# Kernel tuning notes

Hardware: AMD Instinct MI355X
Metric: run time of the kernel (lower is better)

## Reference

```python
import jax, jax.numpy as jnp
import numpy as np

N_NODES = 100000
N_EDGES = 800000
IN_DIM = 128
HIDDEN = 128
CLASSES = 40


def _glorot(key, shape):
    fan_in, fan_out = shape
    lim = (6.0 / (fan_in + fan_out)) ** 0.5
    return jax.random.uniform(key, shape, jnp.float32, -lim, lim)


def setup_inputs() -> dict:
    key = jax.random.key(0)
    ks = jax.random.split(key, 8)
    x = jax.random.normal(ks[0], (N_NODES, IN_DIM), jnp.float32)
    edge_index = jax.random.randint(ks[1], (2, N_EDGES), 0, N_NODES, jnp.int64)
    # SAGEConv layer 1: lin_l (neighbor, with bias), lin_r (root, no bias)
    W1_l = _glorot(ks[2], (IN_DIM, HIDDEN))
    W1_r = _glorot(ks[3], (IN_DIM, HIDDEN))
    b1 = jnp.zeros((HIDDEN,), jnp.float32)
    # SAGEConv layer 2
    W2_l = _glorot(ks[4], (HIDDEN, CLASSES))
    W2_r = _glorot(ks[5], (HIDDEN, CLASSES))
    b2 = jnp.zeros((CLASSES,), jnp.float32)
    return {"x": x, "edge_index": edge_index, "W1_l": W1_l, "W1_r": W1_r,
            "b1": b1, "W2_l": W2_l, "W2_r": W2_r, "b2": b2}


def _sage_conv(x, src, dst, W_l, W_r, b):
    # mean aggregation of source-node features into destination nodes
    msgs = x[src]                                             # [E, d] gather
    agg = jax.ops.segment_sum(msgs, dst, num_segments=N_NODES)  # [N, d]
    cnt = jax.ops.segment_sum(jnp.ones((src.shape[0],), x.dtype), dst,
                              num_segments=N_NODES)           # [N]
    mean = agg / jnp.maximum(cnt, 1.0)[:, None]
    return mean @ W_l + x @ W_r + b


def reference(x, edge_index, W1_l, W1_r, b1, W2_l, W2_r, b2):
    src, dst = edge_index[0], edge_index[1]
    h = _sage_conv(x, src, dst, W1_l, W1_r, b1)
    h = jax.nn.relu(h)
    # F.dropout in eval mode is the identity (deterministic reference)
    out = _sage_conv(h, src, dst, W2_l, W2_r, b2)
    return out
```

## Files before the change

### kernel.cpp

```cpp
#include <hip/hip_runtime.h>
#include <hip/hip_bf16.h>

#define N_NODES 100000
#define N_EDGES 800000
#define IN_DIM  128
#define HIDDEN  128
#define CLASSES 40
#define CAP     32
#define NSH     8
#define SLICES  100
#define EPB     8000
#define BIN_B   (NSH*SLICES)
#define CAST_B  12500
#define PACK_B  24
#define CUR_STRIDE 12544

typedef __attribute__((ext_vector_type(8))) short bf16x8;
typedef __attribute__((ext_vector_type(4))) float floatx4;

__device__ __forceinline__ float bf2f(unsigned short u) {
    return __uint_as_float(((unsigned int)u) << 16);
}
__device__ __forceinline__ unsigned short f2bf(float f) {
    unsigned int u = __float_as_uint(f);
    unsigned int r = 0x7fffu + ((u >> 16) & 1u);
    return (unsigned short)((u + r) >> 16);
}
__device__ __forceinline__ int curIdx(int d) { return (d & 7) * CUR_STRIDE + (d >> 3); }

__global__ void k_prep(const int* __restrict__ src, const int* __restrict__ dst,
                       int* __restrict__ cur, int* __restrict__ csr,
                       const float* __restrict__ x, unsigned short* __restrict__ A1,
                       const float* __restrict__ W1l, const float* __restrict__ W1r,
                       unsigned short* __restrict__ Bp1,
                       const float* __restrict__ W2l, const float* __restrict__ W2r,
                       unsigned short* __restrict__ Bp2) {
    int blk = blockIdx.x;
    if (blk < BIN_B) {
        int g = blk & 7;
        int slice = blk >> 3;
        const int4* s4p = reinterpret_cast<const int4*>(src) + slice * (EPB / 4);
        const int4* d4p = reinterpret_cast<const int4*>(dst) + slice * (EPB / 4);
        for (int i = threadIdx.x; i < EPB / 4; i += 256) {
            int4 d4 = d4p[i];
            int4 s4 = s4p[i];
            #pragma unroll
            for (int j = 0; j < 4; ++j) {
                int d = (&d4.x)[j];
                if ((d & 7) == g) {
                    int s = (&s4.x)[j];
                    int slot = atomicAdd(&cur[g * CUR_STRIDE + (d >> 3)], 1);
                    if (slot < CAP) csr[d * CAP + slot] = s;
                }
            }
        }
    } else if (blk < BIN_B + CAST_B) {
        int t = (blk - BIN_B) * 256 + threadIdx.x;
        int n = t >> 5, g = t & 31;
        float4 v = reinterpret_cast<const float4*>(x + (size_t)n * 128)[g];
        ushort4 u = { f2bf(v.x), f2bf(v.y), f2bf(v.z), f2bf(v.w) };
        *(ushort4*)(A1 + (size_t)n * 256 + 128 + g * 4) = u;
    } else {
        int t = (blk - BIN_B - CAST_B) * 256 + threadIdx.x;
        if (t < 4096) {
            int o = t >> 7, n = t & 127;
            const float* W = (o < 16) ? W1l : W1r;
            int k0 = (o & 15) * 8;
            union { unsigned short us[8]; uint4 v; } pk;
            #pragma unroll
            for (int j = 0; j < 8; ++j) pk.us[j] = f2bf(W[(size_t)(k0 + j) * 128 + n]);
            *(uint4*)(Bp1 + (size_t)t * 8) = pk.v;
        } else {
            int t2 = t - 4096;
            int o = t2 >> 7, n = t2 & 127;
            const float* W = (n < 64) ? W2l : W2r;
            int col = n & 63;
            int k0 = o * 8;
            union { unsigned short us[8]; uint4 v; } pk;
            #pragma unroll
            for (int j = 0; j < 8; ++j)
                pk.us[j] = (col < 40) ? f2bf(W[(size_t)(k0 + j) * 40 + col]) : (unsigned short)0;
            *(uint4*)(Bp2 + (size_t)t2 * 8) = pk.v;
        }
    }
}

__global__ __launch_bounds__(256)
void k_fused(unsigned short* __restrict__ A1, float* __restrict__ Rbuf,
             const int* __restrict__ deg, const int* __restrict__ csr,
             const unsigned short* __restrict__ Bp1, const float* __restrict__ b1,
             const unsigned short* __restrict__ Bp2) {
    __shared__ unsigned short S[4][16][136];
    int wv = threadIdx.x >> 6, lane = threadIdx.x & 63;
    int q = lane >> 4, nn = lane & 15;
    int m0 = blockIdx.x * 64 + wv * 16;

    for (int i = 0; i < 16; i += 2) {
        int nA = m0 + i, nB = m0 + i + 1;
        int aA = min(nA, N_NODES - 1), aB = min(nB, N_NODES - 1);
        int cntA = (nA < N_NODES) ? min(deg[curIdx(aA)], CAP) : 0;
        int cntB = (nB < N_NODES) ? min(deg[curIdx(aB)], CAP) : 0;
        int nl = csr[(lane < 32 ? aA : aB) * CAP + (lane & 31)];
        float accA[8] = {}, accB[8] = {};
        int mx = max(cntA, cntB);
        for (int b = 0; b < mx; b += 16) {
            #pragma unroll
            for (int u = 0; u < 4; ++u) {
                int e = b + u * 4 + q;
                int iA = min(e, cntA - 1) & 31;
                int iB = min(e, cntB - 1) & 31;
                int sA = __shfl(nl, iA, 64);
                int sB = __shfl(nl, 32 + iB, 64);
                bf16x8 vA = {}, vB = {};
                if (e < cntA) vA = *(const bf16x8*)(A1 + (size_t)sA * 256 + 128 + nn * 8);
                if (e < cntB) vB = *(const bf16x8*)(A1 + (size_t)sB * 256 + 128 + nn * 8);
                #pragma unroll
                for (int j = 0; j < 8; ++j) {
                    accA[j] += bf2f((unsigned short)vA[j]);
                    accB[j] += bf2f((unsigned short)vB[j]);
                }
            }
        }
        #pragma unroll
        for (int j = 0; j < 8; ++j) {
            accA[j] += __shfl_xor(accA[j], 16, 64);
            accA[j] += __shfl_xor(accA[j], 32, 64);
            accB[j] += __shfl_xor(accB[j], 16, 64);
            accB[j] += __shfl_xor(accB[j], 32, 64);
        }
        if (lane < 16) {
            float invA = 1.0f / fmaxf((float)cntA, 1.0f);
            float invB = 1.0f / fmaxf((float)cntB, 1.0f);
            union { unsigned short us[8]; bf16x8 v; } pA, pB;
            #pragma unroll
            for (int j = 0; j < 8; ++j) {
                pA.us[j] = f2bf(accA[j] * invA);
                pB.us[j] = f2bf(accB[j] * invB);
            }
            *(bf16x8*)(&S[wv][i][lane * 8])     = pA.v;
            *(bf16x8*)(&S[wv][i + 1][lane * 8]) = pB.v;
        }
    }

    int ma = m0 + nn;
    bool mv = (ma < N_NODES);
    const unsigned short* arow = A1 + (size_t)ma * 256;

    floatx4 acc[8] = {};
    #pragma unroll
    for (int kt = 0; kt < 8; ++kt) {
        bf16x8 a;
        if (kt < 4) {
            a = *(const bf16x8*)(&S[wv][nn][kt * 32 + q * 8]);
        } else {
            a = bf16x8{};
            if (mv) a = *(const bf16x8*)(arow + kt * 32 + q * 8);
        }
        bf16x8 b[8];
        #pragma unroll
        for (int nt = 0; nt < 8; ++nt)
            b[nt] = *(const bf16x8*)(Bp1 + ((size_t)((kt * 4 + q) * 128 + nt * 16 + nn)) * 8);
        #pragma unroll
        for (int nt = 0; nt < 8; ++nt)
            acc[nt] = __builtin_amdgcn_mfma_f32_16x16x32_bf16(a, b[nt], acc[nt], 0, 0, 0);
    }
    #pragma unroll
    for (int nt = 0; nt < 8; ++nt) {
        int col = nt * 16 + nn;
        float bias = b1[col];
        #pragma unroll
        for (int r = 0; r < 4; ++r)
            S[wv][q * 4 + r][col] = f2bf(fmaxf(acc[nt][r] + bias, 0.f));
    }
    floatx4 acc2[8] = {};
    #pragma unroll
    for (int kt = 0; kt < 4; ++kt) {
        bf16x8 a = *(const bf16x8*)(&S[wv][nn][kt * 32 + q * 8]);
        bf16x8 b[8];
        #pragma unroll
        for (int nt = 0; nt < 8; ++nt)
            b[nt] = *(const bf16x8*)(Bp2 + ((size_t)((kt * 4 + q) * 128 + nt * 16 + nn)) * 8);
        #pragma unroll
        for (int nt = 0; nt < 8; ++nt)
            acc2[nt] = __builtin_amdgcn_mfma_f32_16x16x32_bf16(a, b[nt], acc2[nt], 0, 0, 0);
    }
    #pragma unroll
    for (int nt = 0; nt < 4; ++nt) {
        int col = nt * 16 + nn;
        #pragma unroll
        for (int r = 0; r < 4; ++r) {
            int ro = m0 + q * 4 + r;
            if (ro < N_NODES)
                A1[(size_t)ro * 256 + col] = f2bf(acc2[nt][r]);
        }
    }
    #pragma unroll
    for (int nt = 4; nt < 8; ++nt) {
        int col = (nt - 4) * 16 + nn;
        #pragma unroll
        for (int r = 0; r < 4; ++r) {
            int ro = m0 + q * 4 + r;
            if (ro < N_NODES)
                Rbuf[(size_t)ro * 64 + col] = acc2[nt][r];
        }
    }
}

__global__ void k_agg2(const unsigned short* __restrict__ A1, const float* __restrict__ Rbuf,
                       const int* __restrict__ deg, const int* __restrict__ csr,
                       const float* __restrict__ b2, float* __restrict__ out) {
    int pair = blockIdx.x * 4 + (threadIdx.x >> 6);
    int nA = pair * 2, nB = nA + 1;
    int lane = threadIdx.x & 63;
    if (nA >= N_NODES) return;
    int aB = min(nB, N_NODES - 1);
    int cntA = min(deg[curIdx(nA)], CAP);
    int cntB = (nB < N_NODES) ? min(deg[curIdx(aB)], CAP) : 0;
    int nl = csr[(lane < 32 ? nA : aB) * CAP + (lane & 31)];
    int r = lane >> 3, c = lane & 7;
    float accA[8] = {}, accB[8] = {};
    int mx = max(cntA, cntB);
    for (int b = 0; b < mx; b += 16) {
        #pragma unroll
        for (int u = 0; u < 2; ++u) {
            int e = b + u * 8 + r;
            int sA = __shfl(nl, min(e, cntA - 1) & 31, 64);
            int sB = __shfl(nl, 32 + (min(e, cntB - 1) & 31), 64);
            bf16x8 vA = {}, vB = {};
            if (e < cntA) vA = *(const bf16x8*)(A1 + (size_t)sA * 256 + c * 8);
            if (e < cntB) vB = *(const bf16x8*)(A1 + (size_t)sB * 256 + c * 8);
            #pragma unroll
            for (int j = 0; j < 8; ++j) {
                accA[j] += bf2f((unsigned short)vA[j]);
                accB[j] += bf2f((unsigned short)vB[j]);
            }
        }
    }
    #pragma unroll
    for (int j = 0; j < 8; ++j) {
        accA[j] += __shfl_xor(accA[j], 8, 64);
        accA[j] += __shfl_xor(accA[j], 16, 64);
        accA[j] += __shfl_xor(accA[j], 32, 64);
        accB[j] += __shfl_xor(accB[j], 8, 64);
        accB[j] += __shfl_xor(accB[j], 16, 64);
        accB[j] += __shfl_xor(accB[j], 32, 64);
    }
    if (lane < 5) {
        float invA = 1.0f / fmaxf((float)cntA, 1.0f);
        const float* RrowA = Rbuf + (size_t)nA * 64;
        float o[8];
        #pragma unroll
        for (int j = 0; j < 8; ++j)
            o[j] = accA[j] * invA + RrowA[c * 8 + j] + b2[c * 8 + j];
        float* opA = out + (size_t)nA * CLASSES + c * 8;
        *(float4*)(opA)     = make_float4(o[0], o[1], o[2], o[3]);
        *(float4*)(opA + 4) = make_float4(o[4], o[5], o[6], o[7]);
        if (nB < N_NODES) {
            float invB = 1.0f / fmaxf((float)cntB, 1.0f);
            const float* RrowB = Rbuf + (size_t)nB * 64;
            #pragma unroll
            for (int j = 0; j < 8; ++j)
                o[j] = accB[j] * invB + RrowB[c * 8 + j] + b2[c * 8 + j];
            float* opB = out + (size_t)nB * CLASSES + c * 8;
            *(float4*)(opB)     = make_float4(o[0], o[1], o[2], o[3]);
            *(float4*)(opB + 4) = make_float4(o[4], o[5], o[6], o[7]);
        }
    }
}

extern "C" void kernel_launch(void* const* d_in, const int* in_sizes, int n_in,
                              void* d_out, int out_size, void* d_ws, size_t ws_size,
                              hipStream_t stream) {
    const float* x   = (const float*)d_in[0];
    const int*   ei  = (const int*)d_in[1];
    const float* W1l = (const float*)d_in[2];
    const float* W1r = (const float*)d_in[3];
    const float* b1  = (const float*)d_in[4];
    const float* W2l = (const float*)d_in[5];
    const float* W2r = (const float*)d_in[6];
    const float* b2  = (const float*)d_in[7];
    float* out = (float*)d_out;

    const int* src = ei;
    const int* dst = ei + N_EDGES;

    char* ws = (char*)d_ws;
    size_t off = 0;
    auto alloc = [&](size_t bytes) { void* p = ws + off; off += (bytes + 511) & ~(size_t)511; return p; };
    int* cur = (int*)alloc((size_t)NSH * CUR_STRIDE * 4);
    int* csr = (int*)alloc((size_t)N_NODES * CAP * 4);
    unsigned short* Bp1 = (unsigned short*)alloc((size_t)32 * 128 * 8 * 2);
    unsigned short* Bp2 = (unsigned short*)alloc((size_t)16 * 128 * 8 * 2);
    unsigned short* A1  = (unsigned short*)alloc((size_t)N_NODES * 256 * 2);
    float* Rbuf = (float*)alloc((size_t)N_NODES * 64 * 4);

    hipMemsetAsync(cur, 0, (size_t)NSH * CUR_STRIDE * 4, stream);

    k_prep<<<BIN_B + CAST_B + PACK_B, 256, 0, stream>>>(
        src, dst, cur, csr, x, A1, W1l, W1r, Bp1, W2l, W2r, Bp2);

    k_fused<<<(N_NODES + 63) / 64, 256, 0, stream>>>(A1, Rbuf, cur, csr, Bp1, b1, Bp2);
    k_agg2<<<(N_NODES / 2 + 3) / 4, 256, 0, stream>>>(A1, Rbuf, cur, csr, b2, out);
}
```

Before: 281.6 us.

## Split fused aggregation+GEMM into separate agg1 and gemm kernels, reuse A1 for R

Layer-1 neighbor aggregation moves out of the fused kernel into its own k_agg1, which writes the mean into the unused first half of each A1 row. A separate k_gemm then runs both MFMA GEMMs from A1 and stores the root-term output as floats into the upper half of A1, so the separate Rbuf allocation goes away. The binning stage also gets more slices with fewer edges each. The aim is better occupancy and parallelism for the gather phase, which was serialized per wave in the fused kernel, at the cost of an extra launch and an extra round trip of the aggregated features through memory.

Result: faster. 270.2 us (-4.1%).

```diff
diff --git a/kernel.cpp b/kernel.cpp
--- a/kernel.cpp
+++ b/kernel.cpp
@@ -8,8 +8,8 @@
 #define CLASSES 40
 #define CAP     32
 #define NSH     8
-#define SLICES  100
-#define EPB     8000
+#define SLICES  400
+#define EPB     2000
 #define BIN_B   (NSH*SLICES)
 #define CAST_B  12500
 #define PACK_B  24
@@ -85,77 +85,72 @@
     }
 }
 
+__global__ void k_agg1(unsigned short* __restrict__ A1, const int* __restrict__ deg,
+                       const int* __restrict__ csr) {
+    int pair = blockIdx.x * 4 + (threadIdx.x >> 6);
+    int nA = pair * 2, nB = nA + 1;
+    int lane = threadIdx.x & 63;
+    if (nA >= N_NODES) return;
+    int aB = min(nB, N_NODES - 1);
+    int cntA = min(deg[curIdx(nA)], CAP);
+    int cntB = (nB < N_NODES) ? min(deg[curIdx(aB)], CAP) : 0;
+    int nl = csr[(lane < 32 ? nA : aB) * CAP + (lane & 31)];
+    int q = lane >> 4, c = lane & 15;
+    float accA[8] = {}, accB[8] = {};
+    int mx = max(cntA, cntB);
+    for (int b = 0; b < mx; b += 16) {
+        #pragma unroll
+        for (int u = 0; u < 4; ++u) {
+            int e = b + u * 4 + q;
+            int sA = __shfl(nl, min(e, cntA - 1) & 31, 64);
+            int sB = __shfl(nl, 32 + (min(e, cntB - 1) & 31), 64);
+            bf16x8 vA = {}, vB = {};
+            if (e < cntA) vA = *(const bf16x8*)(A1 + (size_t)sA * 256 + 128 + c * 8);
+            if (e < cntB) vB = *(const bf16x8*)(A1 + (size_t)sB * 256 + 128 + c * 8);
+            #pragma unroll
+            for (int j = 0; j < 8; ++j) {
+                accA[j] += bf2f((unsigned short)vA[j]);
+                accB[j] += bf2f((unsigned short)vB[j]);
+            }
+        }
+    }
+    #pragma unroll
+    for (int j = 0; j < 8; ++j) {
+        accA[j] += __shfl_xor(accA[j], 16, 64);
+        accA[j] += __shfl_xor(accA[j], 32, 64);
+        accB[j] += __shfl_xor(accB[j], 16, 64);
+        accB[j] += __shfl_xor(accB[j], 32, 64);
+    }
+    if (lane < 16) {
+        float invA = 1.0f / fmaxf((float)cntA, 1.0f);
+        float invB = 1.0f / fmaxf((float)cntB, 1.0f);
+        union { unsigned short us[8]; bf16x8 v; } pA, pB;
+        #pragma unroll
+        for (int j = 0; j < 8; ++j) {
+            pA.us[j] = f2bf(accA[j] * invA);
+            pB.us[j] = f2bf(accB[j] * invB);
+        }
+        *(bf16x8*)(A1 + (size_t)nA * 256 + c * 8) = pA.v;
+        if (nB < N_NODES)
+            *(bf16x8*)(A1 + (size_t)nB * 256 + c * 8) = pB.v;
+    }
+}
+
 __global__ __launch_bounds__(256)
-void k_fused(unsigned short* __restrict__ A1, float* __restrict__ Rbuf,
-             const int* __restrict__ deg, const int* __restrict__ csr,
-             const unsigned short* __restrict__ Bp1, const float* __restrict__ b1,
-             const unsigned short* __restrict__ Bp2) {
-    __shared__ unsigned short S[4][16][136];
+void k_gemm(unsigned short* __restrict__ A1, const unsigned short* __restrict__ Bp1,
+            const float* __restrict__ b1, const unsigned short* __restrict__ Bp2) {
+    __shared__ unsigned short Hs[4][16][136];
     int wv = threadIdx.x >> 6, lane = threadIdx.x & 63;
     int q = lane >> 4, nn = lane & 15;
     int m0 = blockIdx.x * 64 + wv * 16;
-
-    for (int i = 0; i < 16; i += 2) {
-        int nA = m0 + i, nB = m0 + i + 1;
-        int aA = min(nA, N_NODES - 1), aB = min(nB, N_NODES - 1);
-        int cntA = (nA < N_NODES) ? min(deg[curIdx(aA)], CAP) : 0;
-        int cntB = (nB < N_NODES) ? min(deg[curIdx(aB)], CAP) : 0;
-        int nl = csr[(lane < 32 ? aA : aB) * CAP + (lane & 31)];
-        float accA[8] = {}, accB[8] = {};
-        int mx = max(cntA, cntB);
-        for (int b = 0; b < mx; b += 16) {
-            #pragma unroll
-            for (int u = 0; u < 4; ++u) {
-                int e = b + u * 4 + q;
-                int iA = min(e, cntA - 1) & 31;
-                int iB = min(e, cntB - 1) & 31;
-                int sA = __shfl(nl, iA, 64);
-                int sB = __shfl(nl, 32 + iB, 64);
-                bf16x8 vA = {}, vB = {};
-                if (e < cntA) vA = *(const bf16x8*)(A1 + (size_t)sA * 256 + 128 + nn * 8);
-                if (e < cntB) vB = *(const bf16x8*)(A1 + (size_t)sB * 256 + 128 + nn * 8);
-                #pragma unroll
-                for (int j = 0; j < 8; ++j) {
-                    accA[j] += bf2f((unsigned short)vA[j]);
-                    accB[j] += bf2f((unsigned short)vB[j]);
-                }
-            }
-        }
-        #pragma unroll
-        for (int j = 0; j < 8; ++j) {
-            accA[j] += __shfl_xor(accA[j], 16, 64);
-            accA[j] += __shfl_xor(accA[j], 32, 64);
-            accB[j] += __shfl_xor(accB[j], 16, 64);
-            accB[j] += __shfl_xor(accB[j], 32, 64);
-        }
-        if (lane < 16) {
-            float invA = 1.0f / fmaxf((float)cntA, 1.0f);
-            float invB = 1.0f / fmaxf((float)cntB, 1.0f);
-            union { unsigned short us[8]; bf16x8 v; } pA, pB;
-            #pragma unroll
-            for (int j = 0; j < 8; ++j) {
-                pA.us[j] = f2bf(accA[j] * invA);
-                pB.us[j] = f2bf(accB[j] * invB);
-            }
-            *(bf16x8*)(&S[wv][i][lane * 8])     = pA.v;
-            *(bf16x8*)(&S[wv][i + 1][lane * 8]) = pB.v;
-        }
-    }
-
     int ma = m0 + nn;
     bool mv = (ma < N_NODES);
     const unsigned short* arow = A1 + (size_t)ma * 256;
 
     floatx4 acc[8] = {};
-    #pragma unroll
     for (int kt = 0; kt < 8; ++kt) {
-        bf16x8 a;
-        if (kt < 4) {
-            a = *(const bf16x8*)(&S[wv][nn][kt * 32 + q * 8]);
-        } else {
-            a = bf16x8{};
-            if (mv) a = *(const bf16x8*)(arow + kt * 32 + q * 8);
-        }
+        bf16x8 a = {};
+        if (mv) a = *(const bf16x8*)(arow + kt * 32 + q * 8);
         bf16x8 b[8];
         #pragma unroll
         for (int nt = 0; nt < 8; ++nt)
@@ -170,12 +165,11 @@
         float bias = b1[col];
         #pragma unroll
         for (int r = 0; r < 4; ++r)
-            S[wv][q * 4 + r][col] = f2bf(fmaxf(acc[nt][r] + bias, 0.f));
+            Hs[wv][q * 4 + r][col] = f2bf(fmaxf(acc[nt][r] + bias, 0.f));
     }
     floatx4 acc2[8] = {};
-    #pragma unroll
     for (int kt = 0; kt < 4; ++kt) {
-        bf16x8 a = *(const bf16x8*)(&S[wv][nn][kt * 32 + q * 8]);
+        bf16x8 a = *(const bf16x8*)(&Hs[wv][nn][kt * 32 + q * 8]);
         bf16x8 b[8];
         #pragma unroll
         for (int nt = 0; nt < 8; ++nt)
@@ -200,15 +194,17 @@
         #pragma unroll
         for (int r = 0; r < 4; ++r) {
             int ro = m0 + q * 4 + r;
-            if (ro < N_NODES)
-                Rbuf[(size_t)ro * 64 + col] = acc2[nt][r];
-        }
-    }
-}
-
-__global__ void k_agg2(const unsigned short* __restrict__ A1, const float* __restrict__ Rbuf,
-                       const int* __restrict__ deg, const int* __restrict__ csr,
-                       const float* __restrict__ b2, float* __restrict__ out) {
+            if (ro < N_NODES) {
+                float* Rp = (float*)(A1 + (size_t)ro * 256 + 128);
+                Rp[col] = acc2[nt][r];
+            }
+        }
+    }
+}
+
+__global__ void k_agg2(const unsigned short* __restrict__ A1, const int* __restrict__ deg,
+                       const int* __restrict__ csr, const float* __restrict__ b2,
+                       float* __restrict__ out) {
     int pair = blockIdx.x * 4 + (threadIdx.x >> 6);
     int nA = pair * 2, nB = nA + 1;
     int lane = threadIdx.x & 63;
@@ -247,7 +243,7 @@
     }
     if (lane < 5) {
         float invA = 1.0f / fmaxf((float)cntA, 1.0f);
-        const float* RrowA = Rbuf + (size_t)nA * 64;
+        const float* RrowA = (const float*)(A1 + (size_t)nA * 256 + 128);
         float o[8];
         #pragma unroll
         for (int j = 0; j < 8; ++j)
@@ -257,7 +253,7 @@
         *(float4*)(opA + 4) = make_float4(o[4], o[5], o[6], o[7]);
         if (nB < N_NODES) {
             float invB = 1.0f / fmaxf((float)cntB, 1.0f);
-            const float* RrowB = Rbuf + (size_t)nB * 64;
+            const float* RrowB = (const float*)(A1 + (size_t)nB * 256 + 128);
             #pragma unroll
             for (int j = 0; j < 8; ++j)
                 o[j] = accB[j] * invB + RrowB[c * 8 + j] + b2[c * 8 + j];
@@ -292,13 +288,13 @@
     unsigned short* Bp1 = (unsigned short*)alloc((size_t)32 * 128 * 8 * 2);
     unsigned short* Bp2 = (unsigned short*)alloc((size_t)16 * 128 * 8 * 2);
     unsigned short* A1  = (unsigned short*)alloc((size_t)N_NODES * 256 * 2);
-    float* Rbuf = (float*)alloc((size_t)N_NODES * 64 * 4);
 
     hipMemsetAsync(cur, 0, (size_t)NSH * CUR_STRIDE * 4, stream);
 
     k_prep<<<BIN_B + CAST_B + PACK_B, 256, 0, stream>>>(
         src, dst, cur, csr, x, A1, W1l, W1r, Bp1, W2l, W2r, Bp2);
 
-    k_fused<<<(N_NODES + 63) / 64, 256, 0, stream>>>(A1, Rbuf, cur, csr, Bp1, b1, Bp2);
-    k_agg2<<<(N_NODES / 2 + 3) / 4, 256, 0, stream>>>(A1, Rbuf, cur, csr, b2, out);
-}
+    k_agg1<<<(N_NODES / 2 + 3) / 4, 256, 0, stream>>>(A1, cur, csr);
+    k_gemm<<<(N_NODES + 63) / 64, 256, 0, stream>>>(A1, Bp1, b1, Bp2);
+    k_agg2<<<(N_NODES / 2 + 3) / 4, 256, 0, stream>>>(A1, cur, csr, b2, out);
+}
```
